# Optimization experiments

Measured on AMD Instinct MI355X. Metric: run time of the kernel, lower is better.

Reference implementation:

```python
import jax, jax.numpy as jnp
import numpy as np

B, S, V, E, H, C = 1024, 128, 32000, 512, 1024, 512


def setup_inputs() -> dict:
    key = jax.random.key(0)
    ks = jax.random.split(key, 12)
    x_in = jax.random.randint(ks[0], (B, S), 0, V, dtype=jnp.int32)
    x_lengths = jax.random.randint(ks[1], (B,), 1, S + 1, dtype=jnp.int32)  # in [1, S]

    def nrm(k, shape, scale):
        return jax.random.normal(k, shape, dtype=jnp.float32) * scale

    emb_table = nrm(ks[2], (V, E), 0.02).at[0].set(0.0)  # padding_idx=0 row zeroed
    s_ih = 1.0 / np.sqrt(H)
    W_ih = nrm(ks[3], (H, E), s_ih)
    W_hh = nrm(ks[4], (H, H), s_ih)
    b_ih = nrm(ks[5], (H,), s_ih)
    b_hh = nrm(ks[6], (H,), s_ih)
    W1 = nrm(ks[7], (H, H), 1.0 / np.sqrt(H))
    b1 = nrm(ks[8], (H,), 0.01)
    W2 = nrm(ks[9], (C, H), 1.0 / np.sqrt(H))
    b2 = nrm(ks[10], (C,), 0.01)
    return {
        "x_in": x_in, "x_lengths": x_lengths, "emb_table": emb_table,
        "W_ih": W_ih, "W_hh": W_hh, "b_ih": b_ih, "b_hh": b_hh,
        "W1": W1, "b1": b1, "W2": W2, "b2": b2,
    }


def reference(x_in, x_lengths, emb_table, W_ih, W_hh, b_ih, b_hh, W1, b1, W2, b2):
    # Embedding lookup: (B, S, E)
    x_emb = emb_table[x_in]
    x_seq = jnp.swapaxes(x_emb, 0, 1)  # (S, B, E) for the time scan
    batch = x_in.shape[0]
    h0 = jnp.zeros((batch, W_hh.shape[0]), dtype=x_emb.dtype)

    def step(h, x_t):
        # Elman RNNCell: h' = tanh(x W_ih^T + b_ih + h W_hh^T + b_hh)
        h = jnp.tanh(x_t @ W_ih.T + b_ih + h @ W_hh.T + b_hh)
        return h, h

    _, hs = jax.lax.scan(step, h0, x_seq)  # (S, B, H)
    # column_gather: final hidden at position len-1 per sequence
    y = hs[x_lengths - 1, jnp.arange(batch)]  # (B, H)
    # MLP head (dropout is identity in eval mode)
    y = jax.nn.relu(y @ W1.T + b1)
    return y @ W2.T + b2  # (B, C) logits (apply_softmax=False)
```

## Files before the change

kernel.cpp:

```cpp
#include <hip/hip_runtime.h>

typedef unsigned short u16;
constexpr int Ss = 128, Hn = 1024, En = 512, Cn = 512, Vn = 32000;
constexpr size_t PL = 1024u * 1024u;

using short8 = __attribute__((ext_vector_type(8))) short;
using f32x4  = __attribute__((ext_vector_type(4))) float;

__device__ __align__(1024) u16 g_hh[2][PL];
__device__ __align__(1024) u16 g_hl[2][PL];
__device__ __align__(1024) u16 g_yh[PL], g_yl[PL];
__device__ __align__(1024) u16 g_zh[PL], g_zl[PL];
__device__ __align__(1024) float g_proj[(size_t)Vn * Hn];
__device__ __align__(1024) u16 t_eh[(size_t)Vn * En], t_el[(size_t)Vn * En];
__device__ __align__(1024) u16 t_xh[(size_t)Hn * En], t_xl[(size_t)Hn * En];
__device__ __align__(1024) u16 t_hh[(size_t)Hn * Hn], t_hl[(size_t)Hn * Hn];
__device__ __align__(1024) u16 t_1h[(size_t)Hn * Hn], t_1l[(size_t)Hn * Hn];
__device__ __align__(1024) u16 t_2h[(size_t)Cn * Hn], t_2l[(size_t)Cn * Hn];

__device__ __forceinline__ void gl16(const void* g, void* l) {
  __builtin_amdgcn_global_load_lds((const __attribute__((address_space(1))) void*)g,
                                   (__attribute__((address_space(3))) void*)l, 16, 0, 0);
}
__device__ __forceinline__ unsigned f2bf(float f) {
  unsigned u = __float_as_uint(f);
  return (u + 0x7fffu + ((u >> 16) & 1u)) >> 16;
}
__device__ __forceinline__ float bf2f(unsigned u) { return __uint_as_float(u << 16); }

__global__ void cvt_split(const float* __restrict__ src, int which, int n) {
  u16 *hi, *lo;
  switch (which) {
    case 0: hi = t_eh; lo = t_el; break;
    case 1: hi = t_xh; lo = t_xl; break;
    case 2: hi = t_hh; lo = t_hl; break;
    case 3: hi = t_1h; lo = t_1l; break;
    default: hi = t_2h; lo = t_2l; break;
  }
  for (int i = blockIdx.x * blockDim.x + threadIdx.x; i < n; i += gridDim.x * blockDim.x) {
    const float v = src[i];
    const unsigned h = f2bf(v);
    hi[i] = (u16)h;
    lo[i] = (u16)f2bf(v - bf2f(h));
  }
}

#define GEMM_PROLOG_NOBID()                                                    \
  const int tid = threadIdx.x;                                                 \
  const int w = tid >> 6, l = tid & 63;                                        \
  const int wr = w & 3, wc = w >> 2;                                           \
  const int lrow = l & 15, lk = l >> 4;                                        \
  const int sr = tid >> 3, p = tid & 7;                                        \
  const int sby = ((p ^ (sr & 7)) << 4);                                       \
  const int arow = (wr << 4) + lrow;                                           \
  int aoff[2], bboff[2][2];                                                    \
  _Pragma("unroll") for (int s = 0; s < 2; ++s)                                \
      aoff[s] = arow * 128 + ((s * 64 + lk * 16) ^ ((arow & 7) << 4));         \
  _Pragma("unroll") for (int n = 0; n < 2; ++n) {                              \
    const int jl = (wc << 5) + (n << 4) + lrow;                                \
    _Pragma("unroll") for (int s = 0; s < 2; ++s)                              \
        bboff[n][s] = jl * 128 + ((s * 64 + lk * 16) ^ ((jl & 7) << 4));       \
  }
#define GEMM_PROLOG() const int bid = blockIdx.x; GEMM_PROLOG_NOBID()

#define GEMM_MFMA(ca, cb)                                                      \
  _Pragma("unroll") for (int s = 0; s < 2; ++s) {                              \
    short8 a = *(const short8*)((ca) + aoff[s]);                               \
    _Pragma("unroll") for (int n = 0; n < 2; ++n) {                            \
      short8 b = *(const short8*)((cb) + bboff[n][s]);                         \
      acc[n] = __builtin_amdgcn_mfma_f32_16x16x32_bf16(a, b, acc[n], 0, 0, 0); \
    }                                                                          \
  }

__global__ void __launch_bounds__(512) proj_k(const float* __restrict__ bih,
                                              const float* __restrict__ bhh) {
  __shared__ char ring[65536];
  GEMM_PROLOG()
  const int v0 = (bid % 500) << 6;
  const int j0 = (bid / 500) << 6;

  f32x4 acc[2];
#pragma unroll
  for (int n = 0; n < 2; ++n) {
    const float bs = bih[j0 + (wc << 5) + (n << 4) + lrow] +
                     bhh[j0 + (wc << 5) + (n << 4) + lrow];
#pragma unroll
    for (int ri = 0; ri < 4; ++ri) acc[n][ri] = bs;
  }

  auto stage = [&](int c) {
    char* sl = ring + (c & 1) * 32768;
    const int kb = c * 128;
    gl16((const char*)t_eh + (size_t)(v0 + sr) * 1024 + kb + sby, sl + w * 1024);
    gl16((const char*)t_el + (size_t)(v0 + sr) * 1024 + kb + sby, sl + 8192 + w * 1024);
    gl16((const char*)t_xh + (size_t)(j0 + sr) * 1024 + kb + sby, sl + 16384 + w * 1024);
    gl16((const char*)t_xl + (size_t)(j0 + sr) * 1024 + kb + sby, sl + 24576 + w * 1024);
  };
  stage(0); stage(1);
  for (int c = 0; c < 8; ++c) {
    if (c < 7) asm volatile("s_waitcnt vmcnt(4)" ::: "memory");
    else       asm volatile("s_waitcnt vmcnt(0)" ::: "memory");
    __builtin_amdgcn_s_barrier();
    __builtin_amdgcn_sched_barrier(0);
    const char* sl = ring + (c & 1) * 32768;
#pragma unroll
    for (int s = 0; s < 2; ++s) {
      short8 aH = *(const short8*)(sl + aoff[s]);
      short8 aL = *(const short8*)(sl + 8192 + aoff[s]);
#pragma unroll
      for (int n = 0; n < 2; ++n) {
        short8 bH = *(const short8*)(sl + 16384 + bboff[n][s]);
        short8 bL = *(const short8*)(sl + 24576 + bboff[n][s]);
        acc[n] = __builtin_amdgcn_mfma_f32_16x16x32_bf16(aH, bH, acc[n], 0, 0, 0);
        acc[n] = __builtin_amdgcn_mfma_f32_16x16x32_bf16(aL, bH, acc[n], 0, 0, 0);
        acc[n] = __builtin_amdgcn_mfma_f32_16x16x32_bf16(aH, bL, acc[n], 0, 0, 0);
      }
    }
    __builtin_amdgcn_s_barrier();
    if (c + 2 < 8) stage(c + 2);
  }
#pragma unroll
  for (int n = 0; n < 2; ++n) {
    const int j = j0 + (wc << 5) + (n << 4) + lrow;
#pragma unroll
    for (int ri = 0; ri < 4; ++ri)
      g_proj[(size_t)(v0 + (wr << 4) + lk * 4 + ri) * 1024 + j] = acc[n][ri];
  }
}

__global__ void __launch_bounds__(512) step_k(const int* __restrict__ x_in,
                                              const int* __restrict__ x_len, int t) {
  extern __shared__ char ring[];
  __shared__ int toks[64];
  GEMM_PROLOG()
  const int b0 = (bid & 15) << 6, j0 = (bid >> 4) << 6;
  const u16* hinh = g_hh[t & 1];
  const u16* hinl = g_hl[t & 1];
  u16* houth = g_hh[(t + 1) & 1];
  u16* houtl = g_hl[(t + 1) & 1];

  if (tid < 64) toks[tid] = x_in[(b0 + tid) * Ss + t];
  __syncthreads();

  float pj[2][4];
#pragma unroll
  for (int n = 0; n < 2; ++n) {
    const int j = j0 + (wc << 5) + (n << 4) + lrow;
#pragma unroll
    for (int ri = 0; ri < 4; ++ri)
      pj[n][ri] = g_proj[(size_t)toks[(wr << 4) + lk * 4 + ri] * 1024 + j];
  }
  asm volatile("" ::: "memory");

  f32x4 acc[2];
  acc[0] = (f32x4){0.f, 0.f, 0.f, 0.f}; acc[1] = acc[0];

  if (t > 0) {
    auto stage = [&](int c) {
      char* sl = ring + (c & 3) * 32768;
      const int kb = c * 128;
      gl16((const char*)hinh + (size_t)(b0 + sr) * 2048 + kb + sby, sl + w * 1024);
      gl16((const char*)hinl + (size_t)(b0 + sr) * 2048 + kb + sby, sl + 8192 + w * 1024);
      gl16((const char*)t_hh + (size_t)(j0 + sr) * 2048 + kb + sby, sl + 16384 + w * 1024);
      gl16((const char*)t_hl + (size_t)(j0 + sr) * 2048 + kb + sby, sl + 24576 + w * 1024);
    };
    stage(0); stage(1); stage(2);
    for (int c = 0; c < 16; ++c) {
      const int left = 15 - c;
      if (left >= 2)      asm volatile("s_waitcnt vmcnt(8)" ::: "memory");
      else if (left == 1) asm volatile("s_waitcnt vmcnt(4)" ::: "memory");
      else                asm volatile("s_waitcnt vmcnt(0)" ::: "memory");
      __builtin_amdgcn_s_barrier();
      __builtin_amdgcn_sched_barrier(0);
      if (c + 3 < 16) stage(c + 3);
      const char* sl = ring + (c & 3) * 32768;
#pragma unroll
      for (int s = 0; s < 2; ++s) {
        short8 aH = *(const short8*)(sl + aoff[s]);
        short8 aL = *(const short8*)(sl + 8192 + aoff[s]);
#pragma unroll
        for (int n = 0; n < 2; ++n) {
          short8 bH = *(const short8*)(sl + 16384 + bboff[n][s]);
          short8 bL = *(const short8*)(sl + 24576 + bboff[n][s]);
          acc[n] = __builtin_amdgcn_mfma_f32_16x16x32_bf16(aH, bH, acc[n], 0, 0, 0);
          acc[n] = __builtin_amdgcn_mfma_f32_16x16x32_bf16(aL, bH, acc[n], 0, 0, 0);
          acc[n] = __builtin_amdgcn_mfma_f32_16x16x32_bf16(aH, bL, acc[n], 0, 0, 0);
        }
      }
    }
  }

#pragma unroll
  for (int n = 0; n < 2; ++n) {
    const int j = j0 + (wc << 5) + (n << 4) + lrow;
#pragma unroll
    for (int ri = 0; ri < 4; ++ri) {
      const int brow = b0 + (wr << 4) + lk * 4 + ri;
      const float v = tanhf(acc[n][ri] + pj[n][ri]);
      const unsigned hi = f2bf(v);
      const unsigned lo = f2bf(v - bf2f(hi));
      const size_t off = (size_t)brow * 1024 + j;
      houth[off] = (u16)hi;
      houtl[off] = (u16)lo;
      if (x_len[brow] == t + 1) { g_yh[off] = (u16)hi; g_yl[off] = (u16)lo; }
    }
  }
}

__global__ void __launch_bounds__(512) mlp_k(const float* __restrict__ bias,
                                             float* __restrict__ out, int mode) {
  __shared__ char sA[16384];
  __shared__ char sB[16384];
  GEMM_PROLOG()
  const int b0 = (bid & 15) << 6, j0 = (bid >> 4) << 6;
  const u16* ah = mode ? g_zh : g_yh;
  const u16* al = mode ? g_zl : g_yl;
  const u16* bh = mode ? t_2h : t_1h;
  const u16* bl = mode ? t_2l : t_1l;

  f32x4 acc[2];
#pragma unroll
  for (int n = 0; n < 2; ++n) {
    const float bs = bias[j0 + (wc << 5) + (n << 4) + lrow];
#pragma unroll
    for (int ri = 0; ri < 4; ++ri) acc[n][ri] = bs;
  }

  auto stage = [&](int c) {
    char* da = sA + (c & 1) * 8192;
    char* db = sB + (c & 1) * 8192;
    const u16* ap = (c >= 16 && c < 32) ? al : ah;
    const u16* bp = (c < 32) ? bh : bl;
    const int kb = (c & 15) * 128;
    gl16((const char*)ap + (size_t)(b0 + sr) * 2048 + kb + sby, da + w * 1024);
    gl16((const char*)bp + (size_t)(j0 + sr) * 2048 + kb + sby, db + w * 1024);
  };
  stage(0);
  __syncthreads();
  for (int c = 0; c < 48; ++c) {
    const char* ca = sA + (c & 1) * 8192;
    const char* cb = sB + (c & 1) * 8192;
    if (c < 47) stage(c + 1);
    GEMM_MFMA(ca, cb)
    __syncthreads();
  }

#pragma unroll
  for (int n = 0; n < 2; ++n) {
    const int j = j0 + (wc << 5) + (n << 4) + lrow;
#pragma unroll
    for (int ri = 0; ri < 4; ++ri) {
      const int brow = b0 + (wr << 4) + lk * 4 + ri;
      if (mode == 0) {
        const float v = fmaxf(acc[n][ri], 0.f);
        const unsigned hi = f2bf(v);
        const unsigned lo = f2bf(v - bf2f(hi));
        const size_t off = (size_t)brow * 1024 + j;
        g_zh[off] = (u16)hi;
        g_zl[off] = (u16)lo;
      } else {
        out[(size_t)brow * 512 + j] = acc[n][ri];
      }
    }
  }
}

extern "C" void kernel_launch(void* const* d_in, const int* in_sizes, int n_in,
                              void* d_out, int out_size, void* d_ws, size_t ws_size,
                              hipStream_t stream) {
  const int*   x_in  = (const int*)d_in[0];
  const int*   x_len = (const int*)d_in[1];
  const float* emb = (const float*)d_in[2];
  const float* Wih = (const float*)d_in[3];
  const float* Whh = (const float*)d_in[4];
  const float* bih = (const float*)d_in[5];
  const float* bhh = (const float*)d_in[6];
  const float* W1  = (const float*)d_in[7];
  const float* b1  = (const float*)d_in[8];
  const float* W2  = (const float*)d_in[9];
  const float* b2  = (const float*)d_in[10];
  float* out = (float*)d_out;

  (void)hipFuncSetAttribute((const void*)step_k,
                            hipFuncAttributeMaxDynamicSharedMemorySize, 131072);

  cvt_split<<<dim3(4096), dim3(256), 0, stream>>>(emb, 0, Vn * En);
  cvt_split<<<dim3(1024), dim3(256), 0, stream>>>(Wih, 1, Hn * En);
  cvt_split<<<dim3(2048), dim3(256), 0, stream>>>(Whh, 2, Hn * Hn);
  cvt_split<<<dim3(2048), dim3(256), 0, stream>>>(W1, 3, Hn * Hn);
  cvt_split<<<dim3(1024), dim3(256), 0, stream>>>(W2, 4, Cn * Hn);

  proj_k<<<dim3(8000), dim3(512), 0, stream>>>(bih, bhh);

  for (int t = 0; t < Ss; ++t)
    step_k<<<dim3(256), dim3(512), 131072, stream>>>(x_in, x_len, t);

  mlp_k<<<dim3(256), dim3(512), 0, stream>>>(b1, nullptr, 0);
  mlp_k<<<dim3(128), dim3(512), 0, stream>>>(b2, out, 1);
}
```

Before: 1.731 ms.

## Use 32x32x16 MFMA with split-K across waves in RNN step kernel

The per-timestep recurrent GEMM moves from 16x16x32 MFMA tiles to 32x32x16 tiles. The 8 waves are split into 2 row-groups by 4 K-quarters, and the K-partial sums are reduced through shared memory before the tanh epilogue. The g_proj gather now happens after the reduction instead of being prefetched before the main loop. This cuts MFMA issue count and LDS fragment reads per chunk, at the cost of an extra LDS reduction pass, a block barrier, and losing the early overlap of the projection load.

Result: slower. 2.061 ms (+19.1%).

```diff
diff --git a/kernel.cpp b/kernel.cpp
--- a/kernel.cpp
+++ b/kernel.cpp
@@ -6,6 +6,7 @@
 
 using short8 = __attribute__((ext_vector_type(8))) short;
 using f32x4  = __attribute__((ext_vector_type(4))) float;
+using f32x16 = __attribute__((ext_vector_type(16))) float;
 
 __device__ __align__(1024) u16 g_hh[2][PL];
 __device__ __align__(1024) u16 g_hl[2][PL];
@@ -132,8 +133,25 @@
                                               const int* __restrict__ x_len, int t) {
   extern __shared__ char ring[];
   __shared__ int toks[64];
-  GEMM_PROLOG()
+  const int tid = threadIdx.x, bid = blockIdx.x;
+  const int w = tid >> 6, l = tid & 63;
+  const int sr = tid >> 3, p = tid & 7;
+  const int sby = ((p ^ (sr & 7)) << 4);
   const int b0 = (bid & 15) << 6, j0 = (bid >> 4) << 6;
+
+  const int wp = w >> 2;
+  const int kq = w & 3;
+  const int lr = l & 31, lh = l >> 5;
+  const int ar32 = wp * 32 + lr;
+  const int kfb = kq * 32 + lh * 16;
+  const int aoff32 = ar32 * 128 + (kfb ^ ((ar32 & 7) << 4));
+  int boff32[2];
+#pragma unroll
+  for (int n = 0; n < 2; ++n) {
+    const int jl = n * 32 + lr;
+    boff32[n] = jl * 128 + (kfb ^ ((jl & 7) << 4));
+  }
+
   const u16* hinh = g_hh[t & 1];
   const u16* hinl = g_hl[t & 1];
   u16* houth = g_hh[(t + 1) & 1];
@@ -142,18 +160,11 @@
   if (tid < 64) toks[tid] = x_in[(b0 + tid) * Ss + t];
   __syncthreads();
 
-  float pj[2][4];
-#pragma unroll
-  for (int n = 0; n < 2; ++n) {
-    const int j = j0 + (wc << 5) + (n << 4) + lrow;
-#pragma unroll
-    for (int ri = 0; ri < 4; ++ri)
-      pj[n][ri] = g_proj[(size_t)toks[(wr << 4) + lk * 4 + ri] * 1024 + j];
-  }
-  asm volatile("" ::: "memory");
-
-  f32x4 acc[2];
-  acc[0] = (f32x4){0.f, 0.f, 0.f, 0.f}; acc[1] = acc[0];
+  f32x16 acc[2];
+#pragma unroll
+  for (int n = 0; n < 2; ++n)
+#pragma unroll
+    for (int r = 0; r < 16; ++r) acc[n][r] = 0.f;
 
   if (t > 0) {
     auto stage = [&](int c) {
@@ -174,32 +185,45 @@
       __builtin_amdgcn_sched_barrier(0);
       if (c + 3 < 16) stage(c + 3);
       const char* sl = ring + (c & 3) * 32768;
-#pragma unroll
-      for (int s = 0; s < 2; ++s) {
-        short8 aH = *(const short8*)(sl + aoff[s]);
-        short8 aL = *(const short8*)(sl + 8192 + aoff[s]);
-#pragma unroll
-        for (int n = 0; n < 2; ++n) {
-          short8 bH = *(const short8*)(sl + 16384 + bboff[n][s]);
-          short8 bL = *(const short8*)(sl + 24576 + bboff[n][s]);
-          acc[n] = __builtin_amdgcn_mfma_f32_16x16x32_bf16(aH, bH, acc[n], 0, 0, 0);
-          acc[n] = __builtin_amdgcn_mfma_f32_16x16x32_bf16(aL, bH, acc[n], 0, 0, 0);
-          acc[n] = __builtin_amdgcn_mfma_f32_16x16x32_bf16(aH, bL, acc[n], 0, 0, 0);
-        }
+      short8 aH = *(const short8*)(sl + aoff32);
+      short8 aL = *(const short8*)(sl + 8192 + aoff32);
+#pragma unroll
+      for (int n = 0; n < 2; ++n) {
+        short8 bH = *(const short8*)(sl + 16384 + boff32[n]);
+        short8 bL = *(const short8*)(sl + 24576 + boff32[n]);
+        acc[n] = __builtin_amdgcn_mfma_f32_32x32x16_bf16(aH, bH, acc[n], 0, 0, 0);
+        acc[n] = __builtin_amdgcn_mfma_f32_32x32x16_bf16(aL, bH, acc[n], 0, 0, 0);
+        acc[n] = __builtin_amdgcn_mfma_f32_32x32x16_bf16(aH, bL, acc[n], 0, 0, 0);
       }
     }
   }
 
-#pragma unroll
-  for (int n = 0; n < 2; ++n) {
-    const int j = j0 + (wc << 5) + (n << 4) + lrow;
-#pragma unroll
-    for (int ri = 0; ri < 4; ++ri) {
-      const int brow = b0 + (wr << 4) + lk * 4 + ri;
-      const float v = tanhf(acc[n][ri] + pj[n][ri]);
+  float* part = (float*)ring;
+#pragma unroll
+  for (int n = 0; n < 2; ++n)
+#pragma unroll
+    for (int r = 0; r < 16; ++r)
+      part[(size_t)((w * 2 + n) * 16 + r) * 64 + l] = acc[n][r];
+  __syncthreads();
+
+  const int rp = w >> 2, rq = w & 3;
+#pragma unroll
+  for (int n = 0; n < 2; ++n) {
+    const int jcol = j0 + n * 32 + lr;
+#pragma unroll
+    for (int rr = 0; rr < 4; ++rr) {
+      const int rg = rq * 4 + rr;
+      float s = 0.f;
+#pragma unroll
+      for (int kk = 0; kk < 4; ++kk)
+        s += part[(size_t)(((rp * 4 + kk) * 2 + n) * 16 + rg) * 64 + l];
+      const int lrow2 = (rg & 3) + 8 * (rg >> 2) + 4 * lh;
+      const int brow = b0 + rp * 32 + lrow2;
+      const float pj = g_proj[(size_t)toks[rp * 32 + lrow2] * 1024 + jcol];
+      const float v = tanhf(s + pj);
       const unsigned hi = f2bf(v);
       const unsigned lo = f2bf(v - bf2f(hi));
-      const size_t off = (size_t)brow * 1024 + j;
+      const size_t off = (size_t)brow * 1024 + jcol;
       houth[off] = (u16)hi;
       houtl[off] = (u16)lo;
       if (x_len[brow] == t + 1) { g_yh[off] = (u16)hi; g_yl[off] = (u16)lo; }
```

## Use 256-byte K chunks with double-buffered LDS ring in recurrent step kernel

Applied to the files above, without the earlier changes.

The recurrent step GEMM now stages 256-byte K slices (4 MFMA k-steps) per chunk instead of 128-byte slices. The LDS ring changes from four 32KB buffers with 3-ahead prefetch to two 64KB buffers with 2-ahead prefetch, which halves the number of barrier and wait iterations. The refill for a slot is issued only after a second barrier at the end of each iteration. Addressing is computed inline with an XOR swizzle for the wider rows. This trades prefetch depth and an extra barrier per chunk for fewer, larger transfers.

Result: slower. 2.072 ms (+19.7%).

```diff
diff --git a/kernel.cpp b/kernel.cpp
--- a/kernel.cpp
+++ b/kernel.cpp
@@ -132,8 +132,36 @@
                                               const int* __restrict__ x_len, int t) {
   extern __shared__ char ring[];
   __shared__ int toks[64];
-  GEMM_PROLOG()
+  const int tid = threadIdx.x, bid = blockIdx.x;
+  const int w = tid >> 6, l = tid & 63;
+  const int wr = w & 3, wc = w >> 2;
+  const int lrow = l & 15, lk = l >> 4;
   const int b0 = (bid & 15) << 6, j0 = (bid >> 4) << 6;
+
+  const int arow = (wr << 4) + lrow;
+  int aoff[4], bboff[2][4];
+#pragma unroll
+  for (int s = 0; s < 4; ++s)
+    aoff[s] = arow * 256 + ((s * 64 + lk * 16) ^ ((arow & 7) << 4));
+#pragma unroll
+  for (int n = 0; n < 2; ++n) {
+    const int jl = (wc << 5) + (n << 4) + lrow;
+#pragma unroll
+    for (int s = 0; s < 4; ++s)
+      bboff[n][s] = jl * 256 + ((s * 64 + lk * 16) ^ ((jl & 7) << 4));
+  }
+
+  size_t rbA[2], rbW[2];
+  int dstOff[2];
+#pragma unroll
+  for (int o = 0; o < 2; ++o) {
+    const int row = w * 8 + o * 4 + (l >> 4);
+    const int colb = ((l & 15) ^ (row & 7)) << 4;
+    rbA[o] = (size_t)(b0 + row) * 2048 + colb;
+    rbW[o] = (size_t)(j0 + row) * 2048 + colb;
+    dstOff[o] = (w * 2 + o) * 1024;
+  }
+
   const u16* hinh = g_hh[t & 1];
   const u16* hinl = g_hl[t & 1];
   u16* houth = g_hh[(t + 1) & 1];
@@ -157,36 +185,38 @@
 
   if (t > 0) {
     auto stage = [&](int c) {
-      char* sl = ring + (c & 3) * 32768;
-      const int kb = c * 128;
-      gl16((const char*)hinh + (size_t)(b0 + sr) * 2048 + kb + sby, sl + w * 1024);
-      gl16((const char*)hinl + (size_t)(b0 + sr) * 2048 + kb + sby, sl + 8192 + w * 1024);
-      gl16((const char*)t_hh + (size_t)(j0 + sr) * 2048 + kb + sby, sl + 16384 + w * 1024);
-      gl16((const char*)t_hl + (size_t)(j0 + sr) * 2048 + kb + sby, sl + 24576 + w * 1024);
+      char* sl = ring + (c & 1) * 65536;
+      const size_t ko = (size_t)c * 256;
+#pragma unroll
+      for (int o = 0; o < 2; ++o) {
+        gl16((const char*)hinh + rbA[o] + ko, sl + dstOff[o]);
+        gl16((const char*)hinl + rbA[o] + ko, sl + 16384 + dstOff[o]);
+        gl16((const char*)t_hh + rbW[o] + ko, sl + 32768 + dstOff[o]);
+        gl16((const char*)t_hl + rbW[o] + ko, sl + 49152 + dstOff[o]);
+      }
     };
-    stage(0); stage(1); stage(2);
-    for (int c = 0; c < 16; ++c) {
-      const int left = 15 - c;
-      if (left >= 2)      asm volatile("s_waitcnt vmcnt(8)" ::: "memory");
-      else if (left == 1) asm volatile("s_waitcnt vmcnt(4)" ::: "memory");
-      else                asm volatile("s_waitcnt vmcnt(0)" ::: "memory");
+    stage(0); stage(1);
+    for (int c = 0; c < 8; ++c) {
+      if (c < 7) asm volatile("s_waitcnt vmcnt(8)" ::: "memory");
+      else       asm volatile("s_waitcnt vmcnt(0)" ::: "memory");
       __builtin_amdgcn_s_barrier();
       __builtin_amdgcn_sched_barrier(0);
-      if (c + 3 < 16) stage(c + 3);
-      const char* sl = ring + (c & 3) * 32768;
-#pragma unroll
-      for (int s = 0; s < 2; ++s) {
+      const char* sl = ring + (c & 1) * 65536;
+#pragma unroll
+      for (int s = 0; s < 4; ++s) {
         short8 aH = *(const short8*)(sl + aoff[s]);
-        short8 aL = *(const short8*)(sl + 8192 + aoff[s]);
+        short8 aL = *(const short8*)(sl + 16384 + aoff[s]);
 #pragma unroll
         for (int n = 0; n < 2; ++n) {
-          short8 bH = *(const short8*)(sl + 16384 + bboff[n][s]);
-          short8 bL = *(const short8*)(sl + 24576 + bboff[n][s]);
+          short8 bH = *(const short8*)(sl + 32768 + bboff[n][s]);
+          short8 bL = *(const short8*)(sl + 49152 + bboff[n][s]);
           acc[n] = __builtin_amdgcn_mfma_f32_16x16x32_bf16(aH, bH, acc[n], 0, 0, 0);
           acc[n] = __builtin_amdgcn_mfma_f32_16x16x32_bf16(aL, bH, acc[n], 0, 0, 0);
           acc[n] = __builtin_amdgcn_mfma_f32_16x16x32_bf16(aH, bL, acc[n], 0, 0, 0);
         }
       }
+      __builtin_amdgcn_s_barrier();
+      if (c + 2 < 8) stage(c + 2);
     }
   }
 
```

## Fuse per-timestep RNN launches into one persistent cooperative kernel with grid sync

Applied to the files above, without the earlier changes.

Replaces the 128 separate step kernel launches with a single cooperative kernel that loops over timesteps and uses grid.sync() between steps. Sequence lengths are loaded into registers once instead of being reread every step. The aim is to remove per-launch overhead and the idle gaps between launches. In exchange, all 256 blocks (512 threads, 128KB LDS each) must be co-resident, and each step now pays for a grid-wide barrier.

After: 5.462 ms. 215% more time.

```diff
diff --git a/kernel.cpp b/kernel.cpp
--- a/kernel.cpp
+++ b/kernel.cpp
@@ -1,4 +1,7 @@
 #include <hip/hip_runtime.h>
+#include <hip/hip_cooperative_groups.h>
+
+namespace cg = cooperative_groups;
 
 typedef unsigned short u16;
 constexpr int Ss = 128, Hn = 1024, En = 512, Cn = 512, Vn = 32000;
@@ -128,82 +131,108 @@
   }
 }
 
-__global__ void __launch_bounds__(512) step_k(const int* __restrict__ x_in,
-                                              const int* __restrict__ x_len, int t) {
+__global__ void __launch_bounds__(512) scan_k(const int* __restrict__ x_in,
+                                              const int* __restrict__ x_len) {
+  cg::grid_group grid = cg::this_grid();
   extern __shared__ char ring[];
   __shared__ int toks[64];
-  GEMM_PROLOG()
+  const int tid = threadIdx.x, bid = blockIdx.x;
+  const int w = tid >> 6, l = tid & 63;
+  const int wr = w & 3, wc = w >> 2;
+  const int lrow = l & 15, lk = l >> 4;
+  const int sr = tid >> 3, p = tid & 7;
+  const int sby = ((p ^ (sr & 7)) << 4);
   const int b0 = (bid & 15) << 6, j0 = (bid >> 4) << 6;
-  const u16* hinh = g_hh[t & 1];
-  const u16* hinl = g_hl[t & 1];
-  u16* houth = g_hh[(t + 1) & 1];
-  u16* houtl = g_hl[(t + 1) & 1];
-
-  if (tid < 64) toks[tid] = x_in[(b0 + tid) * Ss + t];
-  __syncthreads();
-
-  float pj[2][4];
-#pragma unroll
-  for (int n = 0; n < 2; ++n) {
-    const int j = j0 + (wc << 5) + (n << 4) + lrow;
-#pragma unroll
-    for (int ri = 0; ri < 4; ++ri)
-      pj[n][ri] = g_proj[(size_t)toks[(wr << 4) + lk * 4 + ri] * 1024 + j];
-  }
-  asm volatile("" ::: "memory");
-
-  f32x4 acc[2];
-  acc[0] = (f32x4){0.f, 0.f, 0.f, 0.f}; acc[1] = acc[0];
-
-  if (t > 0) {
-    auto stage = [&](int c) {
-      char* sl = ring + (c & 3) * 32768;
-      const int kb = c * 128;
-      gl16((const char*)hinh + (size_t)(b0 + sr) * 2048 + kb + sby, sl + w * 1024);
-      gl16((const char*)hinl + (size_t)(b0 + sr) * 2048 + kb + sby, sl + 8192 + w * 1024);
-      gl16((const char*)t_hh + (size_t)(j0 + sr) * 2048 + kb + sby, sl + 16384 + w * 1024);
-      gl16((const char*)t_hl + (size_t)(j0 + sr) * 2048 + kb + sby, sl + 24576 + w * 1024);
-    };
-    stage(0); stage(1); stage(2);
-    for (int c = 0; c < 16; ++c) {
-      const int left = 15 - c;
-      if (left >= 2)      asm volatile("s_waitcnt vmcnt(8)" ::: "memory");
-      else if (left == 1) asm volatile("s_waitcnt vmcnt(4)" ::: "memory");
-      else                asm volatile("s_waitcnt vmcnt(0)" ::: "memory");
-      __builtin_amdgcn_s_barrier();
-      __builtin_amdgcn_sched_barrier(0);
-      if (c + 3 < 16) stage(c + 3);
-      const char* sl = ring + (c & 3) * 32768;
-#pragma unroll
-      for (int s = 0; s < 2; ++s) {
-        short8 aH = *(const short8*)(sl + aoff[s]);
-        short8 aL = *(const short8*)(sl + 8192 + aoff[s]);
-#pragma unroll
-        for (int n = 0; n < 2; ++n) {
-          short8 bH = *(const short8*)(sl + 16384 + bboff[n][s]);
-          short8 bL = *(const short8*)(sl + 24576 + bboff[n][s]);
-          acc[n] = __builtin_amdgcn_mfma_f32_16x16x32_bf16(aH, bH, acc[n], 0, 0, 0);
-          acc[n] = __builtin_amdgcn_mfma_f32_16x16x32_bf16(aL, bH, acc[n], 0, 0, 0);
-          acc[n] = __builtin_amdgcn_mfma_f32_16x16x32_bf16(aH, bL, acc[n], 0, 0, 0);
+
+  const int arow = (wr << 4) + lrow;
+  int aoff[2], bboff[2][2];
+#pragma unroll
+  for (int s = 0; s < 2; ++s)
+    aoff[s] = arow * 128 + ((s * 64 + lk * 16) ^ ((arow & 7) << 4));
+#pragma unroll
+  for (int n = 0; n < 2; ++n) {
+    const int jl = (wc << 5) + (n << 4) + lrow;
+#pragma unroll
+    for (int s = 0; s < 2; ++s)
+      bboff[n][s] = jl * 128 + ((s * 64 + lk * 16) ^ ((jl & 7) << 4));
+  }
+  int lenv[4];
+#pragma unroll
+  for (int ri = 0; ri < 4; ++ri) lenv[ri] = x_len[b0 + (wr << 4) + lk * 4 + ri];
+
+  for (int t = 0; t < Ss; ++t) {
+    const u16* hinh = g_hh[t & 1];
+    const u16* hinl = g_hl[t & 1];
+    u16* houth = g_hh[(t + 1) & 1];
+    u16* houtl = g_hl[(t + 1) & 1];
+
+    if (tid < 64) toks[tid] = x_in[(b0 + tid) * Ss + t];
+    __syncthreads();
+
+    float pj[2][4];
+#pragma unroll
+    for (int n = 0; n < 2; ++n) {
+      const int j = j0 + (wc << 5) + (n << 4) + lrow;
+#pragma unroll
+      for (int ri = 0; ri < 4; ++ri)
+        pj[n][ri] = g_proj[(size_t)toks[(wr << 4) + lk * 4 + ri] * 1024 + j];
+    }
+    asm volatile("" ::: "memory");
+
+    f32x4 acc[2];
+    acc[0] = (f32x4){0.f, 0.f, 0.f, 0.f}; acc[1] = acc[0];
+
+    if (t > 0) {
+      auto stage = [&](int c) {
+        char* sl = ring + (c & 3) * 32768;
+        const int kb = c * 128;
+        gl16((const char*)hinh + (size_t)(b0 + sr) * 2048 + kb + sby, sl + w * 1024);
+        gl16((const char*)hinl + (size_t)(b0 + sr) * 2048 + kb + sby, sl + 8192 + w * 1024);
+        gl16((const char*)t_hh + (size_t)(j0 + sr) * 2048 + kb + sby, sl + 16384 + w * 1024);
+        gl16((const char*)t_hl + (size_t)(j0 + sr) * 2048 + kb + sby, sl + 24576 + w * 1024);
+      };
+      stage(0); stage(1); stage(2);
+      for (int c = 0; c < 16; ++c) {
+        const int left = 15 - c;
+        if (left >= 2)      asm volatile("s_waitcnt vmcnt(8)" ::: "memory");
+        else if (left == 1) asm volatile("s_waitcnt vmcnt(4)" ::: "memory");
+        else                asm volatile("s_waitcnt vmcnt(0)" ::: "memory");
+        __builtin_amdgcn_s_barrier();
+        __builtin_amdgcn_sched_barrier(0);
+        if (c + 3 < 16) stage(c + 3);
+        const char* sl = ring + (c & 3) * 32768;
+#pragma unroll
+        for (int s = 0; s < 2; ++s) {
+          short8 aH = *(const short8*)(sl + aoff[s]);
+          short8 aL = *(const short8*)(sl + 8192 + aoff[s]);
+#pragma unroll
+          for (int n = 0; n < 2; ++n) {
+            short8 bH = *(const short8*)(sl + 16384 + bboff[n][s]);
+            short8 bL = *(const short8*)(sl + 24576 + bboff[n][s]);
+            acc[n] = __builtin_amdgcn_mfma_f32_16x16x32_bf16(aH, bH, acc[n], 0, 0, 0);
+            acc[n] = __builtin_amdgcn_mfma_f32_16x16x32_bf16(aL, bH, acc[n], 0, 0, 0);
+            acc[n] = __builtin_amdgcn_mfma_f32_16x16x32_bf16(aH, bL, acc[n], 0, 0, 0);
+          }
         }
       }
     }
-  }
-
-#pragma unroll
-  for (int n = 0; n < 2; ++n) {
-    const int j = j0 + (wc << 5) + (n << 4) + lrow;
-#pragma unroll
-    for (int ri = 0; ri < 4; ++ri) {
-      const int brow = b0 + (wr << 4) + lk * 4 + ri;
-      const float v = tanhf(acc[n][ri] + pj[n][ri]);
-      const unsigned hi = f2bf(v);
-      const unsigned lo = f2bf(v - bf2f(hi));
-      const size_t off = (size_t)brow * 1024 + j;
-      houth[off] = (u16)hi;
-      houtl[off] = (u16)lo;
-      if (x_len[brow] == t + 1) { g_yh[off] = (u16)hi; g_yl[off] = (u16)lo; }
-    }
+
+#pragma unroll
+    for (int n = 0; n < 2; ++n) {
+      const int j = j0 + (wc << 5) + (n << 4) + lrow;
+#pragma unroll
+      for (int ri = 0; ri < 4; ++ri) {
+        const int brow = b0 + (wr << 4) + lk * 4 + ri;
+        const float v = tanhf(acc[n][ri] + pj[n][ri]);
+        const unsigned hi = f2bf(v);
+        const unsigned lo = f2bf(v - bf2f(hi));
+        const size_t off = (size_t)brow * 1024 + j;
+        houth[off] = (u16)hi;
+        houtl[off] = (u16)lo;
+        if (lenv[ri] == t + 1) { g_yh[off] = (u16)hi; g_yl[off] = (u16)lo; }
+      }
+    }
+    grid.sync();
   }
 }
 
@@ -281,7 +310,7 @@
   const float* b2  = (const float*)d_in[10];
   float* out = (float*)d_out;
 
-  (void)hipFuncSetAttribute((const void*)step_k,
+  (void)hipFuncSetAttribute((const void*)scan_k,
                             hipFuncAttributeMaxDynamicSharedMemorySize, 131072);
 
   cvt_split<<<dim3(4096), dim3(256), 0, stream>>>(emb, 0, Vn * En);
@@ -292,8 +321,9 @@
 
   proj_k<<<dim3(8000), dim3(512), 0, stream>>>(bih, bhh);
 
-  for (int t = 0; t < Ss; ++t)
-    step_k<<<dim3(256), dim3(512), 131072, stream>>>(x_in, x_len, t);
+  void* args[] = {(void*)&x_in, (void*)&x_len};
+  (void)hipLaunchCooperativeKernel((const void*)scan_k, dim3(256), dim3(512),
+                                   args, 131072, stream);
 
   mlp_k<<<dim3(256), dim3(512), 0, stream>>>(b1, nullptr, 0);
   mlp_k<<<dim3(128), dim3(512), 0, stream>>>(b2, out, 1);
```
